# Kernel tuning notes

Hardware: AMD Instinct MI355X
Metric: run time of the kernel (lower is better)

Reference implementation:

```python
import jax, jax.numpy as jnp
import numpy as np

B, T, V = 128, 35, 10000
F, E, H = 1408, 512, 512
R = 81  # 9x9 regions for EfficientNet-b2


def setup_inputs() -> dict:
    key = jax.random.key(0)
    ks = jax.random.split(key, 16)
    s = 0.02
    return {
        "image_features": jax.random.normal(ks[0], (B, R, F), jnp.float32),
        "input_seqs": jax.random.randint(ks[1], (B, T), 0, V),
        "lengths": jax.random.randint(ks[2], (B,), 1, T),
        "emb": jax.random.normal(ks[3], (V, E), jnp.float32) * s,
        "W_ih": jax.random.normal(ks[4], (4 * H, E + F), jnp.float32) * s,
        "b_ih": jnp.zeros((4 * H,), jnp.float32),
        "W_hh": jax.random.normal(ks[5], (4 * H, H), jnp.float32) * s,
        "b_hh": jnp.zeros((4 * H,), jnp.float32),
        "W_init_h": jax.random.normal(ks[6], (H, F), jnp.float32) * s,
        "b_init_h": jnp.zeros((H,), jnp.float32),
        "W_init_c": jax.random.normal(ks[7], (H, F), jnp.float32) * s,
        "b_init_c": jnp.zeros((H,), jnp.float32),
        "W_fc1": jax.random.normal(ks[8], (H, H), jnp.float32) * s,
        "b_fc1": jnp.zeros((H,), jnp.float32),
        "W_fc2": jax.random.normal(ks[9], (V, H), jnp.float32) * s,
        "b_fc2": jnp.zeros((V,), jnp.float32),
    }


def reference(image_features, input_seqs, lengths, emb, W_ih, b_ih, W_hh, b_hh,
              W_init_h, b_init_h, W_init_c, b_init_c, W_fc1, b_fc1, W_fc2, b_fc2):
    # dropout layers are identity in eval mode
    mean_feats = image_features.mean(axis=1)                 # (B, F)
    h0 = jnp.tanh(mean_feats @ W_init_h.T + b_init_h)        # (B, H)
    c0 = jnp.tanh(mean_feats @ W_init_c.T + b_init_c)        # (B, H)
    emb_seq = emb[input_seqs]                                # (B, T, E)
    # precompute input-side gate contributions for all steps (no recurrence needed)
    x_seq = jnp.concatenate(
        [emb_seq, jnp.broadcast_to(mean_feats[:, None, :], (emb_seq.shape[0], emb_seq.shape[1], mean_feats.shape[1]))],
        axis=2)                                              # (B, T, E+F)
    gx_seq = jnp.einsum('bte,ge->btg', x_seq, W_ih) + b_ih + b_hh  # (B, T, 4H)

    def step(carry, gx_t):
        h, c = carry
        gates = gx_t + h @ W_hh.T                            # (B, 4H)
        i, f, g, o = jnp.split(gates, 4, axis=1)
        i, f, o = jax.nn.sigmoid(i), jax.nn.sigmoid(f), jax.nn.sigmoid(o)
        g = jnp.tanh(g)
        c = f * c + i * g
        h = o * jnp.tanh(c)
        out = jax.nn.relu(h @ W_fc1.T + b_fc1)
        logits = out @ W_fc2.T + b_fc2                       # (B, V)
        return (h, c), logits

    _, logits_t = jax.lax.scan(step, (h0, c0), gx_seq.transpose(1, 0, 2))
    return logits_t.transpose(1, 0, 2)                       # (B, T, V)
```

## Files before the change

kernel.cpp:

```cpp
#include <hip/hip_runtime.h>

#define TB 35
#define BB 128
#define VV 10000
#define FF 1408
#define EE 512
#define HH 512
#define G4 2048
#define NBLK 32

typedef unsigned short u16;
typedef unsigned long long u64;
typedef __attribute__((ext_vector_type(8))) short bfrag;
typedef __attribute__((ext_vector_type(4))) float f32x4;

__device__ __forceinline__ u16 f2bf(float f) {
    unsigned u = __float_as_uint(f);
    return (u16)((u + 0x7FFFu + ((u >> 16) & 1u)) >> 16);
}
__device__ __forceinline__ float fast_sig(float x) {
    return __builtin_amdgcn_rcpf(1.f + __expf(-x));
}
__device__ __forceinline__ float fast_tanh(float x) {
    return 1.f - 2.f * __builtin_amdgcn_rcpf(1.f + __expf(2.f * x));
}

__device__ __forceinline__ void gload16(const void* g, void* l) {
    __builtin_amdgcn_global_load_lds(
        (const __attribute__((address_space(1))) void*)g,
        (__attribute__((address_space(3))) void*)l, 16, 0, 0);
}

__global__ __launch_bounds__(256)
void mean_k(const float* __restrict__ img, float* __restrict__ mf) {
    int idx = blockIdx.x * 256 + threadIdx.x;
    int b = idx / FF, f = idx - b * FF;
    const float* p = img + (long)b * (81 * FF) + f;
    float s = 0.f;
    for (int r = 0; r < 81; ++r) s += p[r * FF];
    mf[idx] = s * (1.f / 81.f);
}

__global__ __launch_bounds__(256)
void cast512_k(const float* __restrict__ src, int lds, u16* __restrict__ dst, int n4) {
    int i = blockIdx.x * 256 + threadIdx.x;
    if (i >= n4) return;
    long e = (long)i * 4;
    long row = e >> 9; int col = (int)(e & 511);
    float4 v = *(const float4*)(src + row * lds + col);
    uint2 o;
    o.x = (unsigned)f2bf(v.x) | ((unsigned)f2bf(v.y) << 16);
    o.y = (unsigned)f2bf(v.z) | ((unsigned)f2bf(v.w) << 16);
    *(uint2*)(dst + e) = o;
}

__global__ __launch_bounds__(256)
void init_partial_k(const float* __restrict__ mf,
                    const float* __restrict__ Wh, const float* __restrict__ Wc,
                    const float* __restrict__ Wih,
                    float* __restrict__ part)
{
    __shared__ float As[16][68];
    __shared__ float Ws[16][68];
    const int t  = threadIdx.x;
    const int bx = blockIdx.x;
    const int bm = blockIdx.y * 64;
    const int kz = blockIdx.z;
    const float* W; int ldw; long wr0;
    if (bx < 8)       { W = Wh;       ldw = FF;   wr0 = (long)bx * 64; }
    else if (bx < 16) { W = Wc;       ldw = FF;   wr0 = (long)(bx - 8) * 64; }
    else              { W = Wih + EE; ldw = 1920; wr0 = (long)(bx - 16) * 64; }
    const int lrow = t >> 2, lc4 = (t & 3) << 2;
    const int ty = t >> 4, tx = t & 15;
    const float* arow = mf + (long)(bm + lrow) * FF;
    const float* wrow = W + (wr0 + lrow) * (long)ldw;
    float acc[4][4] = {};
    const int kbeg = kz * 352, kend2 = kbeg + 352;
    for (int k0 = kbeg; k0 < kend2; k0 += 16) {
        float4 av = *(const float4*)(arow + k0 + lc4);
        float4 wv = *(const float4*)(wrow + k0 + lc4);
        As[lc4+0][lrow]=av.x; As[lc4+1][lrow]=av.y; As[lc4+2][lrow]=av.z; As[lc4+3][lrow]=av.w;
        Ws[lc4+0][lrow]=wv.x; Ws[lc4+1][lrow]=wv.y; Ws[lc4+2][lrow]=wv.z; Ws[lc4+3][lrow]=wv.w;
        __syncthreads();
        #pragma unroll
        for (int kk = 0; kk < 16; ++kk) {
            float4 a = *(const float4*)&As[kk][ty*4];
            float4 w = *(const float4*)&Ws[kk][tx*4];
            acc[0][0]+=a.x*w.x; acc[0][1]+=a.x*w.y; acc[0][2]+=a.x*w.z; acc[0][3]+=a.x*w.w;
            acc[1][0]+=a.y*w.x; acc[1][1]+=a.y*w.y; acc[1][2]+=a.y*w.z; acc[1][3]+=a.y*w.w;
            acc[2][0]+=a.z*w.x; acc[2][1]+=a.z*w.y; acc[2][2]+=a.z*w.z; acc[2][3]+=a.z*w.w;
            acc[3][0]+=a.w*w.x; acc[3][1]+=a.w*w.y; acc[3][2]+=a.w*w.z; acc[3][3]+=a.w*w.w;
        }
        __syncthreads();
    }
    const int ncol = bx * 64;
    #pragma unroll
    for (int i = 0; i < 4; ++i) {
        long base = (long)kz * (BB*3072) + (long)(bm + ty*4 + i) * 3072 + ncol + tx*4;
        *(float4*)(part + base) = make_float4(acc[i][0], acc[i][1], acc[i][2], acc[i][3]);
    }
}

__global__ __launch_bounds__(256)
void init_combine_k(const float* __restrict__ part,
                    const float* __restrict__ b_ih, const float* __restrict__ b_hh,
                    const float* __restrict__ b_init_h, const float* __restrict__ b_init_c,
                    u16* __restrict__ h0b, float* __restrict__ c_cur, float* __restrict__ gxb,
                    unsigned* __restrict__ bar)
{
    int idx = blockIdx.x * 256 + threadIdx.x;
    if (idx < 1024) bar[idx] = 0;
    int b = idx / 3072, n = idx - b * 3072;
    float s = part[idx] + part[393216 + idx] + part[2*393216 + idx] + part[3*393216 + idx];
    if (n < 512)       h0b[b*512 + n]         = f2bf(tanhf(s + b_init_h[n]));
    else if (n < 1024) c_cur[b*512 + (n-512)] = tanhf(s + b_init_c[n-512]);
    else               gxb[b*2048 + (n-1024)] = s + b_ih[n-1024] + b_hh[n-1024];
}

template<int ACT, int OBF>
__global__ __launch_bounds__(256)
void gemm_mfma(const u16* __restrict__ A, int lda, const int* __restrict__ rowidx,
               const u16* __restrict__ W, const float* __restrict__ bias,
               const float* __restrict__ radd, int radd_div, int radd_ld,
               void* __restrict__ C, int cdiv, long csq, long csr,
               int mtiles, int N, int K)
{
    __shared__ u16 lA[4096];
    __shared__ u16 lB[4096];
    int bxi, byi;
    if (mtiles > 0) {
        int nwg = gridDim.x, bid = blockIdx.x;
        int q = nwg >> 3, r = nwg & 7;
        int xcd = bid & 7, pos = bid >> 3;
        int lid = (xcd < r) ? (xcd * (q + 1) + pos)
                            : (r * (q + 1) + (xcd - r) * q + pos);
        byi = lid % mtiles;
        bxi = lid / mtiles;
    } else { bxi = blockIdx.x; byi = blockIdx.y; }

    const int t    = threadIdx.x;
    const int bm   = byi * 128;
    const int bn   = bxi * 128;
    const int lane = t & 63;
    const int wv   = t >> 6;
    const int wm   = (wv >> 1) * 64;
    const int wn   = (wv & 1) * 64;
    const int fr   = lane & 15;
    const int cc   = lane >> 4;

    const int q0 = t, q1 = t + 256;
    const int ra0 = q0 >> 2, ca0 = (q0 & 3) ^ ((ra0 >> 1) & 3);
    const int ra1 = q1 >> 2, ca1 = (q1 & 3) ^ ((ra1 >> 1) & 3);
    long arow0 = rowidx ? (long)rowidx[bm + ra0] : (long)(bm + ra0);
    long arow1 = rowidx ? (long)rowidx[bm + ra1] : (long)(bm + ra1);
    const u16* asrc0 = A + arow0 * lda + ca0 * 8;
    const u16* asrc1 = A + arow1 * lda + ca1 * 8;
    int brow0 = bn + ra0; if (brow0 > N - 1) brow0 = N - 1;
    int brow1 = bn + ra1; if (brow1 > N - 1) brow1 = N - 1;
    const u16* bsrc0 = W + (long)brow0 * K + ca0 * 8;
    const u16* bsrc1 = W + (long)brow1 * K + ca1 * 8;
    u16* adst0 = lA + q0 * 8;  u16* adst1 = lA + q1 * 8;
    u16* bdst0 = lB + q0 * 8;  u16* bdst1 = lB + q1 * 8;

    int aoff[4], boff[4];
    #pragma unroll
    for (int i = 0; i < 4; ++i) {
        int rA = wm + i * 16 + fr;
        aoff[i] = rA * 64 + ((cc ^ ((rA >> 1) & 3)) << 4);
        int rB = wn + i * 16 + fr;
        boff[i] = rB * 64 + ((cc ^ ((rB >> 1) & 3)) << 4);
    }
    const char* lac = (const char*)lA;
    const char* lbc = (const char*)lB;

    f32x4 acc[4][4] = {};
    for (int k0 = 0; k0 < K; k0 += 32) {
        gload16(asrc0 + k0, adst0);
        gload16(asrc1 + k0, adst1);
        gload16(bsrc0 + k0, bdst0);
        gload16(bsrc1 + k0, bdst1);
        __syncthreads();
        bfrag av[4], bv[4];
        #pragma unroll
        for (int i = 0; i < 4; ++i) av[i] = *(const bfrag*)(lac + aoff[i]);
        #pragma unroll
        for (int i = 0; i < 4; ++i) bv[i] = *(const bfrag*)(lbc + boff[i]);
        #pragma unroll
        for (int mi = 0; mi < 4; ++mi)
            #pragma unroll
            for (int ni = 0; ni < 4; ++ni)
                acc[mi][ni] = __builtin_amdgcn_mfma_f32_16x16x32_bf16(
                    av[mi], bv[ni], acc[mi][ni], 0, 0, 0);
        __syncthreads();
    }

    #pragma unroll
    for (int mi = 0; mi < 4; ++mi) {
        #pragma unroll
        for (int r = 0; r < 4; ++r) {
            int m = bm + wm + mi * 16 + (lane >> 4) * 4 + r;
            long cb = (long)(m / cdiv) * csq + (long)(m % cdiv) * csr;
            const float* rr = radd ? (radd + (long)(m / radd_div) * radd_ld) : nullptr;
            #pragma unroll
            for (int ni = 0; ni < 4; ++ni) {
                int n = bn + wn + ni * 16 + fr;
                if (n < N) {
                    float v = acc[mi][ni][r];
                    if (bias) v += bias[n];
                    if (rr)   v += rr[n];
                    if (ACT == 2) v = fmaxf(v, 0.f);
                    if (OBF) ((u16*)C)[cb + n] = f2bf(v);
                    else     ((float*)C)[cb + n] = v;
                }
            }
        }
    }
}

__global__ __launch_bounds__(256, 1)
void lstm_rec_k(const u16* __restrict__ h0b, const float* __restrict__ c0,
                const float* __restrict__ Whh, const float* __restrict__ gx,
                u16* __restrict__ h_b, unsigned* __restrict__ bar)
{
    __shared__ bfrag Wf[4096];
    const int t256 = threadIdx.x;
    const int jb   = blockIdx.x;
    const int lane = t256 & 63;
    const int w    = t256 >> 6;
    const int fr   = lane & 15;
    const int cc   = lane >> 4;

    for (int q = 0; q < 16; ++q) {
        int flat = t256 + q * 256;
        int r = flat >> 6, kg = flat & 63;
        int mi = r >> 4, jj = r & 15;
        int kk = kg >> 2, c2 = kg & 3;
        const float* src = Whh + (long)(mi * 512 + jb * 16 + jj) * 512 + kg * 8;
        float4 s0 = *(const float4*)src;
        float4 s1 = *(const float4*)(src + 4);
        bfrag p;
        p[0] = (short)f2bf(s0.x); p[1] = (short)f2bf(s0.y);
        p[2] = (short)f2bf(s0.z); p[3] = (short)f2bf(s0.w);
        p[4] = (short)f2bf(s1.x); p[5] = (short)f2bf(s1.y);
        p[6] = (short)f2bf(s1.z); p[7] = (short)f2bf(s1.w);
        Wf[(kk * 4 + mi) * 64 + c2 * 16 + jj] = p;
    }

    const int b0   = w * 32 + fr;
    const int jcol = jb * 16 + cc * 4;

    f32x4 creg[2];
    #pragma unroll
    for (int ni = 0; ni < 2; ++ni)
        creg[ni] = *(const f32x4*)(c0 + (long)(b0 + ni*16) * 512 + jcol);

    f32x4 gxc[4][2];
    #pragma unroll
    for (int ni = 0; ni < 2; ++ni) {
        const float* gp = gx + (long)(b0 + ni*16) * G4 + jcol;
        #pragma unroll
        for (int g = 0; g < 4; ++g) gxc[g][ni] = *(const f32x4*)(gp + g * 512);
    }

    __syncthreads();

    const u16* hsrc = h0b;
    for (int t = 0; t < TB; ++t) {
        bfrag hreg[2][16];
        #pragma unroll
        for (int ni = 0; ni < 2; ++ni) {
            const u16* hp = hsrc + (long)(b0 + ni*16) * 512 + cc * 8;
            #pragma unroll
            for (int kk = 0; kk < 16; ++kk)
                hreg[ni][kk] = *(const bfrag*)(hp + kk * 32);
        }

        f32x4 acc[4][2] = {};
        #pragma unroll
        for (int kk = 0; kk < 16; ++kk) {
            bfrag av0 = Wf[(kk*4 + 0) * 64 + lane];
            bfrag av1 = Wf[(kk*4 + 1) * 64 + lane];
            bfrag av2 = Wf[(kk*4 + 2) * 64 + lane];
            bfrag av3 = Wf[(kk*4 + 3) * 64 + lane];
            #pragma unroll
            for (int ni = 0; ni < 2; ++ni) {
                acc[0][ni] = __builtin_amdgcn_mfma_f32_16x16x32_bf16(av0, hreg[ni][kk], acc[0][ni], 0,0,0);
                acc[1][ni] = __builtin_amdgcn_mfma_f32_16x16x32_bf16(av1, hreg[ni][kk], acc[1][ni], 0,0,0);
                acc[2][ni] = __builtin_amdgcn_mfma_f32_16x16x32_bf16(av2, hreg[ni][kk], acc[2][ni], 0,0,0);
                acc[3][ni] = __builtin_amdgcn_mfma_f32_16x16x32_bf16(av3, hreg[ni][kk], acc[3][ni], 0,0,0);
            }
        }

        u16* hd = h_b + (long)t * (BB*HH);
        #pragma unroll
        for (int ni = 0; ni < 2; ++ni) {
            u64 hq = 0;
            #pragma unroll
            for (int rr = 0; rr < 4; ++rr) {
                float ig = fast_sig (acc[0][ni][rr] + gxc[0][ni][rr]);
                float fg = fast_sig (acc[1][ni][rr] + gxc[1][ni][rr]);
                float gg = fast_tanh(acc[2][ni][rr] + gxc[2][ni][rr]);
                float og = fast_sig (acc[3][ni][rr] + gxc[3][ni][rr]);
                float c  = fg * creg[ni][rr] + ig * gg;
                creg[ni][rr] = c;
                hq |= (u64)f2bf(og * fast_tanh(c)) << (rr * 16);
            }
            __hip_atomic_store((u64*)(hd + (long)(b0 + ni*16) * 512 + jcol), hq,
                               __ATOMIC_RELAXED, __HIP_MEMORY_SCOPE_AGENT);
        }
        hsrc = hd;

        if (t < TB - 1) {
            f32x4 gxn[4][2];
            #pragma unroll
            for (int ni = 0; ni < 2; ++ni) {
                const float* gp = gx + ((long)(t+1) * BB + b0 + ni*16) * G4 + jcol;
                #pragma unroll
                for (int g = 0; g < 4; ++g) gxn[g][ni] = *(const f32x4*)(gp + g * 512);
            }
            __syncthreads();
            if (t256 == 0) {
                unsigned* ctr = bar + t * 16;
                __hip_atomic_fetch_add(ctr, 1u, __ATOMIC_RELAXED, __HIP_MEMORY_SCOPE_AGENT);
                while (__hip_atomic_load(ctr, __ATOMIC_RELAXED, __HIP_MEMORY_SCOPE_AGENT) < NBLK)
                    __builtin_amdgcn_s_sleep(2);
            }
            __syncthreads();
            __builtin_amdgcn_fence(__ATOMIC_ACQUIRE, "agent");
            #pragma unroll
            for (int g = 0; g < 4; ++g)
                #pragma unroll
                for (int ni = 0; ni < 2; ++ni) gxc[g][ni] = gxn[g][ni];
        }
    }
}

extern "C" void kernel_launch(void* const* d_in, const int* in_sizes, int n_in,
                              void* d_out, int out_size, void* d_ws, size_t ws_size,
                              hipStream_t stream)
{
    const float* img    = (const float*)d_in[0];
    const int*   seqs   = (const int*)d_in[1];
    const float* emb    = (const float*)d_in[3];
    const float* W_ih   = (const float*)d_in[4];
    const float* b_ih   = (const float*)d_in[5];
    const float* W_hh   = (const float*)d_in[6];
    const float* b_hh   = (const float*)d_in[7];
    const float* W_inh  = (const float*)d_in[8];
    const float* b_inh  = (const float*)d_in[9];
    const float* W_inc  = (const float*)d_in[10];
    const float* b_inc  = (const float*)d_in[11];
    const float* W_fc1  = (const float*)d_in[12];
    const float* b_fc1  = (const float*)d_in[13];
    const float* W_fc2  = (const float*)d_in[14];
    const float* b_fc2  = (const float*)d_in[15];
    float* out = (float*)d_out;

    float*    ws  = (float*)d_ws;
    unsigned* bar = (unsigned*)ws;
    float* mf    = ws    + 1024;
    float* c_cur = mf    + 180224;
    float* gxb   = c_cur + 65536;
    float* gx    = gxb   + 262144;
    float* ipart = gx;
    u16*   h_b    = (u16*)(gx + 9175040);
    u16*   h0b    = h_b    + 2293760;
    u16*   emb_b  = h0b    + 65536;
    u16*   wih_b  = emb_b  + 5120000;
    u16*   wfc1_b = wih_b  + 1048576;
    u16*   wfc2_b = wfc1_b + 262144;
    u16*   o_b    = wfc2_b + 5120000;

    cast512_k<<<5000, 256, 0, stream>>>(emb,   512,  emb_b,  1280000);
    cast512_k<<<1024, 256, 0, stream>>>(W_ih,  1920, wih_b,   262144);
    cast512_k<<< 256, 256, 0, stream>>>(W_fc1, 512,  wfc1_b,   65536);
    cast512_k<<<5000, 256, 0, stream>>>(W_fc2, 512,  wfc2_b, 1280000);

    mean_k<<<704, 256, 0, stream>>>(img, mf);
    init_partial_k<<<dim3(48, 2, 4), 256, 0, stream>>>(mf, W_inh, W_inc, W_ih, ipart);
    init_combine_k<<<1536, 256, 0, stream>>>(ipart, b_ih, b_hh, b_inh, b_inc,
                                             h0b, c_cur, gxb, bar);

    gemm_mfma<0,0><<<dim3(16 * 35), 256, 0, stream>>>(emb_b, EE, seqs, wih_b, nullptr,
                                                      gxb, TB, G4, gx, TB, G4,
                                                      (long)BB * G4, 35, G4, EE);

    lstm_rec_k<<<dim3(NBLK), dim3(256), 0, stream>>>(h0b, c_cur, W_hh, gx, h_b, bar);

    gemm_mfma<2,1><<<dim3(4, 35), 256, 0, stream>>>(h_b, HH, nullptr, wfc1_b, b_fc1,
                                                    nullptr, 1, 0, o_b, 1 << 30, 0, HH,
                                                    0, HH, HH);
    gemm_mfma<0,0><<<dim3(79 * 35), 256, 0, stream>>>(o_b, HH, nullptr, wfc2_b, b_fc2,
                                                      nullptr, 1, 0, out, BB, VV,
                                                      (long)TB * VV, 35, VV, HH);
}
```

Measured before the change: 557.4 us.

## Fuse LSTM recurrence with fc1/fc2 GEMMs in a persistent producer-consumer kernel

Replaces the separate recurrence, fc1 and fc2 launches with one 288-block persistent kernel. Thirty-two blocks run the recurrence, 32 blocks compute fc1 per timestep once that step's flag counter shows completion, and 224 blocks compute fc2 tiles once the fc1 counter for the step is complete. The intent is to overlap the output projection with the serial recurrence instead of running it afterwards. This depends on all blocks being co-resident and on the bar counters (including offset 600) being zeroed. Spin-waits and a less tuned tile GEMM may reduce throughput on the large fc2 projection.

```diff
diff --git a/kernel.cpp b/kernel.cpp
--- a/kernel.cpp
+++ b/kernel.cpp
@@ -217,120 +217,247 @@
     }
 }
 
-__global__ __launch_bounds__(256, 1)
-void lstm_rec_k(const u16* __restrict__ h0b, const float* __restrict__ c0,
-                const float* __restrict__ Whh, const float* __restrict__ gx,
-                u16* __restrict__ h_b, unsigned* __restrict__ bar)
+template<int ACT, int OBF>
+__device__ __forceinline__ void tile_gemm(u16* shm, const u16* Abase, const u16* W,
+                                          int bn, int N, const float* bias,
+                                          char* Cbase, long crs )
 {
-    __shared__ bfrag Wf[4096];
-    const int t256 = threadIdx.x;
-    const int jb   = blockIdx.x;
-    const int lane = t256 & 63;
-    const int w    = t256 >> 6;
+    u16* lA = shm;
+    u16* lB = shm + 4096;
+    const int t    = threadIdx.x;
+    const int lane = t & 63;
+    const int wv   = t >> 6;
+    const int wm   = (wv >> 1) * 64;
+    const int wn   = (wv & 1) * 64;
     const int fr   = lane & 15;
     const int cc   = lane >> 4;
 
-    for (int q = 0; q < 16; ++q) {
-        int flat = t256 + q * 256;
-        int r = flat >> 6, kg = flat & 63;
-        int mi = r >> 4, jj = r & 15;
-        int kk = kg >> 2, c2 = kg & 3;
-        const float* src = Whh + (long)(mi * 512 + jb * 16 + jj) * 512 + kg * 8;
-        float4 s0 = *(const float4*)src;
-        float4 s1 = *(const float4*)(src + 4);
-        bfrag p;
-        p[0] = (short)f2bf(s0.x); p[1] = (short)f2bf(s0.y);
-        p[2] = (short)f2bf(s0.z); p[3] = (short)f2bf(s0.w);
-        p[4] = (short)f2bf(s1.x); p[5] = (short)f2bf(s1.y);
-        p[6] = (short)f2bf(s1.z); p[7] = (short)f2bf(s1.w);
-        Wf[(kk * 4 + mi) * 64 + c2 * 16 + jj] = p;
-    }
-
-    const int b0   = w * 32 + fr;
-    const int jcol = jb * 16 + cc * 4;
-
-    f32x4 creg[2];
+    const int q0 = t, q1 = t + 256;
+    const int ra0 = q0 >> 2, ca0 = (q0 & 3) ^ ((ra0 >> 1) & 3);
+    const int ra1 = q1 >> 2, ca1 = (q1 & 3) ^ ((ra1 >> 1) & 3);
+    const u16* asrc0 = Abase + (long)ra0 * 512 + ca0 * 8;
+    const u16* asrc1 = Abase + (long)ra1 * 512 + ca1 * 8;
+    int brow0 = bn + ra0; if (brow0 > N - 1) brow0 = N - 1;
+    int brow1 = bn + ra1; if (brow1 > N - 1) brow1 = N - 1;
+    const u16* bsrc0 = W + (long)brow0 * 512 + ca0 * 8;
+    const u16* bsrc1 = W + (long)brow1 * 512 + ca1 * 8;
+    u16* adst0 = lA + q0 * 8;  u16* adst1 = lA + q1 * 8;
+    u16* bdst0 = lB + q0 * 8;  u16* bdst1 = lB + q1 * 8;
+
+    int aoff[4], boff[4];
     #pragma unroll
-    for (int ni = 0; ni < 2; ++ni)
-        creg[ni] = *(const f32x4*)(c0 + (long)(b0 + ni*16) * 512 + jcol);
-
-    f32x4 gxc[4][2];
+    for (int i = 0; i < 4; ++i) {
+        int rA = wm + i * 16 + fr;
+        aoff[i] = rA * 64 + ((cc ^ ((rA >> 1) & 3)) << 4);
+        int rB = wn + i * 16 + fr;
+        boff[i] = 8192 + rB * 64 + ((cc ^ ((rB >> 1) & 3)) << 4);
+    }
+    const char* lc = (const char*)lA;
+
+    f32x4 acc[4][4] = {};
+    for (int k0 = 0; k0 < 512; k0 += 32) {
+        gload16(asrc0 + k0, adst0);
+        gload16(asrc1 + k0, adst1);
+        gload16(bsrc0 + k0, bdst0);
+        gload16(bsrc1 + k0, bdst1);
+        __syncthreads();
+        bfrag av[4], bv[4];
+        #pragma unroll
+        for (int i = 0; i < 4; ++i) av[i] = *(const bfrag*)(lc + aoff[i]);
+        #pragma unroll
+        for (int i = 0; i < 4; ++i) bv[i] = *(const bfrag*)(lc + boff[i]);
+        #pragma unroll
+        for (int mi = 0; mi < 4; ++mi)
+            #pragma unroll
+            for (int ni = 0; ni < 4; ++ni)
+                acc[mi][ni] = __builtin_amdgcn_mfma_f32_16x16x32_bf16(
+                    av[mi], bv[ni], acc[mi][ni], 0, 0, 0);
+        __syncthreads();
+    }
+
     #pragma unroll
-    for (int ni = 0; ni < 2; ++ni) {
-        const float* gp = gx + (long)(b0 + ni*16) * G4 + jcol;
-        #pragma unroll
-        for (int g = 0; g < 4; ++g) gxc[g][ni] = *(const f32x4*)(gp + g * 512);
-    }
-
-    __syncthreads();
-
-    const u16* hsrc = h0b;
-    for (int t = 0; t < TB; ++t) {
-        bfrag hreg[2][16];
+    for (int mi = 0; mi < 4; ++mi) {
+        #pragma unroll
+        for (int r = 0; r < 4; ++r) {
+            int m = wm + mi * 16 + (lane >> 4) * 4 + r;
+            char* crow = Cbase + (long)m * crs;
+            #pragma unroll
+            for (int ni = 0; ni < 4; ++ni) {
+                int n = bn + wn + ni * 16 + fr;
+                if (n < N) {
+                    float v = acc[mi][ni][r] + bias[n];
+                    if (ACT == 2) v = fmaxf(v, 0.f);
+                    if (OBF)
+                        __hip_atomic_store((u16*)crow + n, f2bf(v),
+                                           __ATOMIC_RELAXED, __HIP_MEMORY_SCOPE_AGENT);
+                    else
+                        __builtin_nontemporal_store(v, (float*)crow + n);
+                }
+            }
+        }
+    }
+}
+
+__global__ __launch_bounds__(256, 1)
+void mega_k(const u16* __restrict__ h0b, const float* __restrict__ c0,
+            const float* __restrict__ Whh, const float* __restrict__ gx,
+            u16* __restrict__ h_b, unsigned* __restrict__ bar,
+            const u16* __restrict__ wfc1, const float* __restrict__ b_fc1,
+            u16* __restrict__ o_b,
+            const u16* __restrict__ wfc2, const float* __restrict__ b_fc2,
+            float* __restrict__ out)
+{
+    __shared__ alignas(16) u16 shm[32768];
+    const int bid  = blockIdx.x;
+    const int t256 = threadIdx.x;
+    const int lane = t256 & 63;
+
+    if (bid < NBLK) {
+        bfrag* Wf = (bfrag*)shm;
+        const int jb = bid;
+        const int w  = t256 >> 6;
+        const int fr = lane & 15;
+        const int cc = lane >> 4;
+
+        for (int q = 0; q < 16; ++q) {
+            int flat = t256 + q * 256;
+            int r = flat >> 6, kg = flat & 63;
+            int mi = r >> 4, jj = r & 15;
+            int kk = kg >> 2, c2 = kg & 3;
+            const float* src = Whh + (long)(mi * 512 + jb * 16 + jj) * 512 + kg * 8;
+            float4 s0 = *(const float4*)src;
+            float4 s1 = *(const float4*)(src + 4);
+            bfrag p;
+            p[0] = (short)f2bf(s0.x); p[1] = (short)f2bf(s0.y);
+            p[2] = (short)f2bf(s0.z); p[3] = (short)f2bf(s0.w);
+            p[4] = (short)f2bf(s1.x); p[5] = (short)f2bf(s1.y);
+            p[6] = (short)f2bf(s1.z); p[7] = (short)f2bf(s1.w);
+            Wf[(kk * 4 + mi) * 64 + c2 * 16 + jj] = p;
+        }
+
+        const int b0   = w * 32 + fr;
+        const int jcol = jb * 16 + cc * 4;
+
+        f32x4 creg[2];
+        #pragma unroll
+        for (int ni = 0; ni < 2; ++ni)
+            creg[ni] = *(const f32x4*)(c0 + (long)(b0 + ni*16) * 512 + jcol);
+
+        f32x4 gxc[4][2];
         #pragma unroll
         for (int ni = 0; ni < 2; ++ni) {
-            const u16* hp = hsrc + (long)(b0 + ni*16) * 512 + cc * 8;
-            #pragma unroll
-            for (int kk = 0; kk < 16; ++kk)
-                hreg[ni][kk] = *(const bfrag*)(hp + kk * 32);
-        }
-
-        f32x4 acc[4][2] = {};
-        #pragma unroll
-        for (int kk = 0; kk < 16; ++kk) {
-            bfrag av0 = Wf[(kk*4 + 0) * 64 + lane];
-            bfrag av1 = Wf[(kk*4 + 1) * 64 + lane];
-            bfrag av2 = Wf[(kk*4 + 2) * 64 + lane];
-            bfrag av3 = Wf[(kk*4 + 3) * 64 + lane];
+            const float* gp = gx + (long)(b0 + ni*16) * G4 + jcol;
+            #pragma unroll
+            for (int g = 0; g < 4; ++g) gxc[g][ni] = *(const f32x4*)(gp + g * 512);
+        }
+
+        __syncthreads();
+
+        const u16* hsrc = h0b;
+        for (int t = 0; t < TB; ++t) {
+            bfrag hreg[2][16];
             #pragma unroll
             for (int ni = 0; ni < 2; ++ni) {
-                acc[0][ni] = __builtin_amdgcn_mfma_f32_16x16x32_bf16(av0, hreg[ni][kk], acc[0][ni], 0,0,0);
-                acc[1][ni] = __builtin_amdgcn_mfma_f32_16x16x32_bf16(av1, hreg[ni][kk], acc[1][ni], 0,0,0);
-                acc[2][ni] = __builtin_amdgcn_mfma_f32_16x16x32_bf16(av2, hreg[ni][kk], acc[2][ni], 0,0,0);
-                acc[3][ni] = __builtin_amdgcn_mfma_f32_16x16x32_bf16(av3, hreg[ni][kk], acc[3][ni], 0,0,0);
-            }
-        }
-
-        u16* hd = h_b + (long)t * (BB*HH);
-        #pragma unroll
-        for (int ni = 0; ni < 2; ++ni) {
-            u64 hq = 0;
-            #pragma unroll
-            for (int rr = 0; rr < 4; ++rr) {
-                float ig = fast_sig (acc[0][ni][rr] + gxc[0][ni][rr]);
-                float fg = fast_sig (acc[1][ni][rr] + gxc[1][ni][rr]);
-                float gg = fast_tanh(acc[2][ni][rr] + gxc[2][ni][rr]);
-                float og = fast_sig (acc[3][ni][rr] + gxc[3][ni][rr]);
-                float c  = fg * creg[ni][rr] + ig * gg;
-                creg[ni][rr] = c;
-                hq |= (u64)f2bf(og * fast_tanh(c)) << (rr * 16);
-            }
-            __hip_atomic_store((u64*)(hd + (long)(b0 + ni*16) * 512 + jcol), hq,
-                               __ATOMIC_RELAXED, __HIP_MEMORY_SCOPE_AGENT);
-        }
-        hsrc = hd;
-
-        if (t < TB - 1) {
-            f32x4 gxn[4][2];
+                const u16* hp = hsrc + (long)(b0 + ni*16) * 512 + cc * 8;
+                #pragma unroll
+                for (int kk = 0; kk < 16; ++kk)
+                    hreg[ni][kk] = *(const bfrag*)(hp + kk * 32);
+            }
+
+            f32x4 acc[4][2] = {};
+            #pragma unroll
+            for (int kk = 0; kk < 16; ++kk) {
+                bfrag av0 = Wf[(kk*4 + 0) * 64 + lane];
+                bfrag av1 = Wf[(kk*4 + 1) * 64 + lane];
+                bfrag av2 = Wf[(kk*4 + 2) * 64 + lane];
+                bfrag av3 = Wf[(kk*4 + 3) * 64 + lane];
+                #pragma unroll
+                for (int ni = 0; ni < 2; ++ni) {
+                    acc[0][ni] = __builtin_amdgcn_mfma_f32_16x16x32_bf16(av0, hreg[ni][kk], acc[0][ni], 0,0,0);
+                    acc[1][ni] = __builtin_amdgcn_mfma_f32_16x16x32_bf16(av1, hreg[ni][kk], acc[1][ni], 0,0,0);
+                    acc[2][ni] = __builtin_amdgcn_mfma_f32_16x16x32_bf16(av2, hreg[ni][kk], acc[2][ni], 0,0,0);
+                    acc[3][ni] = __builtin_amdgcn_mfma_f32_16x16x32_bf16(av3, hreg[ni][kk], acc[3][ni], 0,0,0);
+                }
+            }
+
+            u16* hd = h_b + (long)t * (BB*HH);
             #pragma unroll
             for (int ni = 0; ni < 2; ++ni) {
-                const float* gp = gx + ((long)(t+1) * BB + b0 + ni*16) * G4 + jcol;
+                u64 hq = 0;
                 #pragma unroll
-                for (int g = 0; g < 4; ++g) gxn[g][ni] = *(const f32x4*)(gp + g * 512);
-            }
-            __syncthreads();
+                for (int rr = 0; rr < 4; ++rr) {
+                    float ig = fast_sig (acc[0][ni][rr] + gxc[0][ni][rr]);
+                    float fg = fast_sig (acc[1][ni][rr] + gxc[1][ni][rr]);
+                    float gg = fast_tanh(acc[2][ni][rr] + gxc[2][ni][rr]);
+                    float og = fast_sig (acc[3][ni][rr] + gxc[3][ni][rr]);
+                    float c  = fg * creg[ni][rr] + ig * gg;
+                    creg[ni][rr] = c;
+                    hq |= (u64)f2bf(og * fast_tanh(c)) << (rr * 16);
+                }
+                __hip_atomic_store((u64*)(hd + (long)(b0 + ni*16) * 512 + jcol), hq,
+                                   __ATOMIC_RELAXED, __HIP_MEMORY_SCOPE_AGENT);
+            }
+            hsrc = hd;
+
+            if (t < TB - 1) {
+                f32x4 gxn[4][2];
+                #pragma unroll
+                for (int ni = 0; ni < 2; ++ni) {
+                    const float* gp = gx + ((long)(t+1) * BB + b0 + ni*16) * G4 + jcol;
+                    #pragma unroll
+                    for (int g = 0; g < 4; ++g) gxn[g][ni] = *(const f32x4*)(gp + g * 512);
+                }
+                __syncthreads();
+                if (t256 == 0) {
+                    unsigned* ctr = bar + t * 16;
+                    __hip_atomic_fetch_add(ctr, 1u, __ATOMIC_RELAXED, __HIP_MEMORY_SCOPE_AGENT);
+                    while (__hip_atomic_load(ctr, __ATOMIC_RELAXED, __HIP_MEMORY_SCOPE_AGENT) < NBLK)
+                        __builtin_amdgcn_s_sleep(2);
+                }
+                __syncthreads();
+                __builtin_amdgcn_fence(__ATOMIC_ACQUIRE, "agent");
+                #pragma unroll
+                for (int g = 0; g < 4; ++g)
+                    #pragma unroll
+                    for (int ni = 0; ni < 2; ++ni) gxc[g][ni] = gxn[g][ni];
+            } else {
+                __syncthreads();
+                if (t256 == 0)
+                    __hip_atomic_fetch_add(bar + t * 16, 1u,
+                                           __ATOMIC_RELAXED, __HIP_MEMORY_SCOPE_AGENT);
+            }
+        }
+    } else if (bid < 64) {
+        const int wkr = bid - 32;
+        for (int g = wkr; g < TB * 4; g += 32) {
+            int tt = g >> 2, nt4 = g & 3;
             if (t256 == 0) {
-                unsigned* ctr = bar + t * 16;
-                __hip_atomic_fetch_add(ctr, 1u, __ATOMIC_RELAXED, __HIP_MEMORY_SCOPE_AGENT);
-                while (__hip_atomic_load(ctr, __ATOMIC_RELAXED, __HIP_MEMORY_SCOPE_AGENT) < NBLK)
-                    __builtin_amdgcn_s_sleep(2);
+                while (__hip_atomic_load(bar + tt * 16, __ATOMIC_RELAXED,
+                                         __HIP_MEMORY_SCOPE_AGENT) < NBLK)
+                    __builtin_amdgcn_s_sleep(10);
             }
             __syncthreads();
             __builtin_amdgcn_fence(__ATOMIC_ACQUIRE, "agent");
-            #pragma unroll
-            for (int g = 0; g < 4; ++g)
-                #pragma unroll
-                for (int ni = 0; ni < 2; ++ni) gxc[g][ni] = gxn[g][ni];
+            tile_gemm<2,1>(shm, h_b + (long)tt * (BB*HH), wfc1, nt4 * 128, HH, b_fc1,
+                           (char*)(o_b + (long)tt * (BB*HH)), HH * 2);
+            __syncthreads();
+            if (t256 == 0)
+                __hip_atomic_fetch_add(bar + 600 + tt, 1u,
+                                       __ATOMIC_RELAXED, __HIP_MEMORY_SCOPE_AGENT);
+        }
+    } else {
+        const int wkr = bid - 64;
+        for (int g = wkr; g < TB * 79; g += 224) {
+            int tt = g / 79, nt = g - tt * 79;
+            if (t256 == 0) {
+                while (__hip_atomic_load(bar + 600 + tt, __ATOMIC_RELAXED,
+                                         __HIP_MEMORY_SCOPE_AGENT) < 4)
+                    __builtin_amdgcn_s_sleep(10);
+            }
+            __syncthreads();
+            __builtin_amdgcn_fence(__ATOMIC_ACQUIRE, "agent");
+            tile_gemm<0,0>(shm, o_b + (long)tt * (BB*HH), wfc2, nt * 128, VV, b_fc2,
+                           (char*)(out + (long)tt * VV), (long)TB * VV * 4);
         }
     }
 }
@@ -385,12 +512,6 @@
                                                       gxb, TB, G4, gx, TB, G4,
                                                       (long)BB * G4, 35, G4, EE);
 
-    lstm_rec_k<<<dim3(NBLK), dim3(256), 0, stream>>>(h0b, c_cur, W_hh, gx, h_b, bar);
-
-    gemm_mfma<2,1><<<dim3(4, 35), 256, 0, stream>>>(h_b, HH, nullptr, wfc1_b, b_fc1,
-                                                    nullptr, 1, 0, o_b, 1 << 30, 0, HH,
-                                                    0, HH, HH);
-    gemm_mfma<0,0><<<dim3(79 * 35), 256, 0, stream>>>(o_b, HH, nullptr, wfc2_b, b_fc2,
-                                                      nullptr, 1, 0, out, BB, VV,
-                                                      (long)TB * VV, 35, VV, HH);
-}
+    mega_k<<<dim3(288), dim3(256), 0, stream>>>(h0b, c_cur, W_hh, gx, h_b, bar,
+                                                wfc1_b, b_fc1, o_b, wfc2_b, b_fc2, out);
+}
```

After: 556.5 us. About the same (-0.2%).
